# Performance work log

Hardware: AMD Instinct MI355X
Metric: run time of the kernel (lower is better)

## Reference

```python
import jax, jax.numpy as jnp
import numpy as np

N, C, MH, MW = 128, 256, 28, 28
K = 80          # num_classes
P = 196         # cfg.num_points
SH, SW = 200, 200  # stride-4 semantic feature map
STRIDE = 4.0
FC_IN = C + 2 * K  # 416


def _bilinear(feat, px, py):
    # feat: (C,H,W); px,py: (N,P) pixel coords. grid_sample semantics:
    # align_corners=False, zero padding.
    _, H, W = feat.shape
    x0 = jnp.floor(px); y0 = jnp.floor(py)
    wx1 = px - x0; wy1 = py - y0
    def corner(xc, yc, w):
        valid = (xc >= 0) & (xc <= W - 1) & (yc >= 0) & (yc <= H - 1)
        xi = jnp.clip(xc, 0, W - 1).astype(jnp.int32)
        yi = jnp.clip(yc, 0, H - 1).astype(jnp.int32)
        return feat[:, yi, xi] * (w * valid)[None]  # (C,N,P)
    out = (corner(x0, y0, (1 - wx1) * (1 - wy1)) + corner(x0 + 1, y0, wx1 * (1 - wy1))
           + corner(x0, y0 + 1, (1 - wx1) * wy1) + corner(x0 + 1, y0 + 1, wx1 * wy1))
    return jnp.transpose(out, (1, 0, 2))  # (N,C,P)


def setup_inputs():
    key = jax.random.key(0)
    ks = jax.random.split(key, 16)
    s = 0.02
    instance_feats = jax.random.normal(ks[0], (N, C, MH, MW), jnp.float32)
    semantic_feat = jax.random.normal(ks[1], (1, C, SH, SW), jnp.float32)
    img_w, img_h = SW * STRIDE, SH * STRIDE
    x1 = jax.random.uniform(ks[2], (N,)) * (img_w * 0.5)
    y1 = jax.random.uniform(ks[3], (N,)) * (img_h * 0.5)
    bw = 32.0 + jax.random.uniform(ks[4], (N,)) * (img_w * 0.4)
    bh = 32.0 + jax.random.uniform(ks[5], (N,)) * (img_h * 0.4)
    rois = jnp.stack([jnp.zeros((N,)), x1, y1,
                      jnp.minimum(x1 + bw, img_w - 1),
                      jnp.minimum(y1 + bh, img_h - 1)], axis=1)
    roi_labels = jax.random.randint(ks[6], (N,), 0, K)
    return dict(
        instance_feats=instance_feats, semantic_feat=semantic_feat, rois=rois,
        roi_labels=roi_labels, num_points=P,
        w_sem=s * jax.random.normal(ks[7], (C, C)), b_sem=jnp.zeros((C,)),
        w_inst=s * jax.random.normal(ks[8], (K, C)), b_inst=jnp.zeros((K,)),
        w_det=s * jax.random.normal(ks[9], (K, C)), b_det=jnp.zeros((K,)),
        fc_w0=s * jax.random.normal(ks[10], (C, FC_IN)), fc_b0=jnp.zeros((C,)),
        fc_w1=s * jax.random.normal(ks[11], (C, FC_IN)), fc_b1=jnp.zeros((C,)),
        fc_w2=s * jax.random.normal(ks[12], (C, FC_IN)), fc_b2=jnp.zeros((C,)),
        w_logits=s * jax.random.normal(ks[13], (C, FC_IN)), b_logits=jnp.zeros((C,)),
        w_fuse=s * jax.random.normal(ks[14], (C, C)), b_fuse=jnp.zeros((C,)))


def reference(instance_feats, semantic_feat, rois, roi_labels, num_points,
              w_sem, b_sem, w_inst, b_inst, w_det, b_det,
              fc_w0, fc_b0, fc_w1, fc_b1, fc_w2, fc_b2,
              w_logits, b_logits, w_fuse, b_fuse):
    n, c, mh, mw = instance_feats.shape
    hw = mh * mw
    sem = jax.nn.relu(jnp.einsum('bchw,oc->bohw', semantic_feat, w_sem) + b_sem[None, :, None, None])
    inst_log = jnp.einsum('nchw,oc->nohw', instance_feats, w_inst) + b_inst[None, :, None, None]
    det_log = jnp.einsum('nchw,oc->nohw', instance_feats, w_det) + b_det[None, :, None, None]
    ridx = jnp.arange(n)
    instance_preds = inst_log[ridx, roi_labels][:, None]  # (n,1,mh,mw) class-selected
    detail_preds = det_log[ridx, roi_labels][:, None]
    # top-k uncertain-point selection on the (detached) detail map
    point_map = jax.lax.stop_gradient(detail_preds.reshape(n, hw))
    _, point_indices = jax.lax.top_k(point_map, num_points)  # (n,P)
    rel_x = ((point_indices % mw).astype(jnp.float32) + 0.5) / mw
    rel_y = ((point_indices // mw).astype(jnp.float32) + 0.5) / mh
    # roi-relative [0,1]^2 -> semantic feature map pixel coords (align_corners=False)
    px = (rois[:, 1:2] + rel_x * (rois[:, 3:4] - rois[:, 1:2])) / STRIDE - 0.5
    py = (rois[:, 2:3] + rel_y * (rois[:, 4:5] - rois[:, 2:3])) / STRIDE - 0.5
    fine = _bilinear(sem[0], px, py)  # (n,C,P); all rois belong to image 0
    k = inst_log.shape[1]
    idx = jnp.broadcast_to(point_indices[:, None, :], (n, k, point_indices.shape[1]))
    c_inst = jnp.take_along_axis(inst_log.reshape(n, k, hw), idx, axis=2)  # (n,K,P)
    c_det = jnp.take_along_axis(det_log.reshape(n, k, hw), idx, axis=2)
    x = jnp.concatenate([fine, c_inst, c_det], axis=1)  # (n, C+2K, P)
    for w_, b_ in ((fc_w0, fc_b0), (fc_w1, fc_b1), (fc_w2, fc_b2)):
        x = jax.nn.relu(jnp.einsum('ncp,oc->nop', x, w_) + b_[None, :, None])
        x = jnp.concatenate([x, c_inst, c_det], axis=1)
    pts = jnp.einsum('ncp,oc->nop', x, w_logits) + b_logits[None, :, None]  # (n,C,P)
    coarse = instance_feats.reshape(n, c, hw)
    refined = coarse.at[ridx[:, None, None], jnp.arange(c)[None, :, None],
                        point_indices[:, None, :]].set(pts)
    refined = refined.reshape(n, c, mh, mw)
    fused = jax.nn.relu(jnp.einsum('nchw,oc->nohw', refined, w_fuse) + b_fuse[None, :, None, None])
    up = jax.image.resize(fused, (n, c, 2 * mh, 2 * mw), method='bilinear')
    return instance_preds, detail_preds, jax.nn.relu(up)
```

## Files before the change

### kernel.cpp

```cpp
#include <hip/hip_runtime.h>

#define NN   128
#define CC   256
#define MH   28
#define MW   28
#define HW   784
#define KCLS 80
#define PP   196
#define SHH  200
#define SWW  200
#define SPIX 40000
#define FCIN 416

typedef __attribute__((ext_vector_type(8))) short short8;
typedef __attribute__((ext_vector_type(4))) float f32x4;

__device__ __forceinline__ unsigned short f2bf(float x) {
  unsigned u = __float_as_uint(x);
  unsigned r = (u + 0x7fffu + ((u >> 16) & 1u)) >> 16;
  return (unsigned short)r;
}
__device__ __forceinline__ float bf2f(unsigned short h) {
  return __uint_as_float((unsigned)h << 16);
}

#define OW_SEM  0
#define OW_FUSE 65536
#define OW_FC0  131072
#define OW_FC1  237568
#define OW_FC2  344064
#define OW_LOG  450560
#define OW_CAT  557056
#define OW_TOT  598016
__global__ void wconv_k(const float* __restrict__ wsem, const float* __restrict__ wfuse,
                        const float* __restrict__ w0, const float* __restrict__ w1,
                        const float* __restrict__ w2, const float* __restrict__ wlog,
                        const float* __restrict__ wi, const float* __restrict__ wd,
                        const float* __restrict__ bi, const float* __restrict__ bd,
                        unsigned short* __restrict__ out, float* __restrict__ bcat) {
  const int tid0 = blockIdx.x * blockDim.x + threadIdx.x;
  if (tid0 < KCLS) bcat[tid0] = bi[tid0];
  else if (tid0 < 2 * KCLS) bcat[tid0] = bd[tid0 - KCLS];
  for (int i = tid0; i < OW_TOT; i += gridDim.x * blockDim.x) {
    float v;
    if (i < OW_FUSE) v = wsem[i];
    else if (i < OW_FC0) v = wfuse[i - OW_FUSE];
    else if (i < OW_FC1) v = w0[i - OW_FC0];
    else if (i < OW_FC2) v = w1[i - OW_FC1];
    else if (i < OW_LOG) v = w2[i - OW_FC2];
    else if (i < OW_CAT) v = wlog[i - OW_LOG];
    else if (i < OW_CAT + KCLS * 256) v = wi[i - OW_CAT];
    else v = wd[i - OW_CAT - KCLS * 256];
    out[i] = f2bf(v);
  }
}

__global__ __launch_bounds__(256) void transpose_bf16_k(
    const float* __restrict__ src, unsigned short* __restrict__ dst, int P) {
  __shared__ float T[64][69];
  const int t = threadIdx.x;
  src += (size_t)blockIdx.z * 256 * P;
  dst += (size_t)blockIdx.z * P * 256;
  const int p0 = blockIdx.x * 64, c0 = blockIdx.y * 64;
#pragma unroll
  for (int it = 0; it < 16; ++it) {
    int idx = it * 256 + t, c = idx >> 6, p = idx & 63;
    T[c][p] = (p0 + p < P) ? src[(size_t)(c0 + c) * P + p0 + p] : 0.f;
  }
  __syncthreads();
#pragma unroll
  for (int it = 0; it < 16; ++it) {
    int idx = it * 256 + t, p = idx >> 6, c = idx & 63;
    if (p0 + p < P) dst[(size_t)(p0 + p) * 256 + c0 + c] = f2bf(T[c][p]);
  }
}

template <int ASRC, int EPI>
__global__ __launch_bounds__(256) void gemm_mfma_k(
    const void* __restrict__ Ap, const unsigned short* __restrict__ Bmat,
    const float* __restrict__ bias, float* __restrict__ outf,
    unsigned short* __restrict__ outh, const int* __restrict__ pidx,
    int M, int N, int K, int lda, int ldb) {
  __shared__ __align__(16) unsigned short Abuf[128 * 40];
  __shared__ __align__(16) unsigned short Bbuf[128 * 40];
  const int t = threadIdx.x;
  const int m0 = blockIdx.x * 128, n0 = blockIdx.y * 128;
  if (EPI == 3) {
    Bmat += (size_t)blockIdx.z * HW * 256;
    outf += (size_t)blockIdx.z * CC * HW;
  }
  const unsigned short* Ah = (const unsigned short*)Ap;
  const int wave = t >> 6, lane = t & 63, lq = lane >> 4, lr = lane & 15;
  const int msub = (wave & 1) * 64, nsub = (wave >> 1) * 64;
  f32x4 acc[4][4] = {};
  for (int kc = 0; kc < K; kc += 32) {
#pragma unroll
    for (int it = 0; it < 4; ++it) {
      const int idx = it * 256 + t, r = idx >> 3, jg = idx & 7;
      const int gm = m0 + r;
      ushort4 h = make_ushort4(0, 0, 0, 0);
      if (gm < M) h = *(const ushort4*)&Ah[(size_t)gm * lda + kc + jg * 4];
      *(ushort4*)&Abuf[r * 40 + jg * 4] = h;
    }
#pragma unroll
    for (int it = 0; it < 4; ++it) {
      const int idx = it * 256 + t, r = idx >> 3, jg = idx & 7;
      const int gn = n0 + r;
      ushort4 h = make_ushort4(0, 0, 0, 0);
      if (gn < N) h = *(const ushort4*)&Bmat[(size_t)gn * ldb + kc + jg * 4];
      *(ushort4*)&Bbuf[r * 40 + jg * 4] = h;
    }
    __syncthreads();
    short8 af[4], bfr[4];
#pragma unroll
    for (int i = 0; i < 4; ++i)
      af[i] = *(const short8*)&Abuf[(msub + i * 16 + lr) * 40 + lq * 8];
#pragma unroll
    for (int f = 0; f < 4; ++f)
      bfr[f] = *(const short8*)&Bbuf[(nsub + f * 16 + lr) * 40 + lq * 8];
#pragma unroll
    for (int i = 0; i < 4; ++i)
#pragma unroll
      for (int f = 0; f < 4; ++f)
        acc[i][f] = __builtin_amdgcn_mfma_f32_16x16x32_bf16(af[i], bfr[f],
                                                            acc[i][f], 0, 0, 0);
    __syncthreads();
  }
#pragma unroll
  for (int i = 0; i < 4; ++i) {
#pragma unroll
    for (int r = 0; r < 4; ++r) {
      const int gm = m0 + msub + i * 16 + lq * 4 + r;
      if (EPI == 3) {
        const float bb = bias[gm];
#pragma unroll
        for (int f = 0; f < 4; ++f) {
          const int gs = n0 + nsub + f * 16 + lr;
          if (gs < N) outf[(size_t)gm * HW + gs] = fmaxf(acc[i][f][r] + bb, 0.f);
        }
      } else if (EPI == 4) {
        if (gm < M) {
#pragma unroll
          for (int f = 0; f < 4; ++f) {
            const int go = n0 + nsub + f * 16 + lr;
            outh[(size_t)gm * 256 + go] = f2bf(fmaxf(acc[i][f][r] + bias[go], 0.f));
          }
        }
      }
    }
  }
}

#define XRS 424
__global__ __launch_bounds__(256) void fused_point_k(
    const unsigned short* __restrict__ semh,
    unsigned short* __restrict__ refined_t,
    const int* __restrict__ pidx, const float* __restrict__ rois,
    const unsigned short* __restrict__ wbf, const float* __restrict__ bcat,
    const float* __restrict__ fb0, const float* __restrict__ fb1,
    const float* __restrict__ fb2, const float* __restrict__ bl) {
  __shared__ __align__(16) unsigned short X[64 * XRS];
  __shared__ int rowoff[64];
  __shared__ float pxs[64], pys[64];
  const int t = threadIdx.x;
  const int gm0 = blockIdx.x * 64;
  const int lane = t & 63, wave = t >> 6, lq = lane >> 4, lr = lane & 15;
  if (t < 64) {
    const int gm = gm0 + t;
    const int n = gm / PP;
    const int si = pidx[gm];
    rowoff[t] = (n * HW + si) * 256;
    const float rx = ((float)(si % MW) + 0.5f) / (float)MW;
    const float ry = ((float)(si / MW) + 0.5f) / (float)MH;
    const float x1 = rois[n * 5 + 1], y1 = rois[n * 5 + 2];
    const float x2 = rois[n * 5 + 3], y2 = rois[n * 5 + 4];
    pxs[t] = (x1 + rx * (x2 - x1)) * 0.25f - 0.5f;
    pys[t] = (y1 + ry * (y2 - y1)) * 0.25f - 0.5f;
  }
  __syncthreads();
  {
    const int c0 = (t & 31) * 8;
    const int rbase = t >> 5;
#pragma unroll
    for (int it = 0; it < 8; ++it) {
      const int r = it * 8 + rbase;
      const float px = pxs[r], py = pys[r];
      const float x0f = floorf(px), y0f = floorf(py);
      const int x0 = (int)x0f, y0 = (int)y0f;
      const float wx1 = px - x0f, wy1 = py - y0f;
      float out[8] = {};
#pragma unroll
      for (int cy = 0; cy < 2; ++cy) {
        const int yy = y0 + cy;
        const bool vy = (yy >= 0) && (yy <= SHH - 1);
        const int yc = min(max(yy, 0), SHH - 1);
        const float wy = cy ? wy1 : (1.f - wy1);
#pragma unroll
        for (int cx = 0; cx < 2; ++cx) {
          const int xx = x0 + cx;
          const bool vx = (xx >= 0) && (xx <= SWW - 1);
          const int xc = min(max(xx, 0), SWW - 1);
          const float wgt = (vx && vy) ? wy * (cx ? wx1 : (1.f - wx1)) : 0.f;
          const unsigned short* src = semh + ((size_t)yc * SWW + xc) * 256 + c0;
          short8 v = *(const short8*)src;
#pragma unroll
          for (int j = 0; j < 8; ++j) out[j] += wgt * bf2f((unsigned short)v[j]);
        }
      }
      short8 o;
#pragma unroll
      for (int j = 0; j < 8; ++j) o[j] = (short)f2bf(out[j]);
      *(short8*)&X[r * XRS + c0] = o;
    }
  }
  {
    const int grow = rowoff[wave * 16 + lr];
    const unsigned short* Wc = wbf + OW_CAT;
    f32x4 acc[10] = {};
    for (int kc = 0; kc < 256; kc += 32) {
      const short8 a = *(const short8*)&refined_t[(size_t)grow + kc + lq * 8];
#pragma unroll
      for (int f = 0; f < 10; ++f) {
        const short8 b = *(const short8*)&Wc[(size_t)(f * 16 + lr) * 256 + kc + lq * 8];
        acc[f] = __builtin_amdgcn_mfma_f32_16x16x32_bf16(a, b, acc[f], 0, 0, 0);
      }
    }
#pragma unroll
    for (int f = 0; f < 10; ++f) {
      const int col = 256 + f * 16 + lr;
      const float bb = bcat[f * 16 + lr];
#pragma unroll
      for (int r = 0; r < 4; ++r) {
        const int row = wave * 16 + lq * 4 + r;
        X[row * XRS + col] = f2bf(acc[f][r] + bb);
      }
    }
  }
  __syncthreads();
  const int n0w = wave * 64;
  for (int layer = 0; layer < 4; ++layer) {
    const unsigned short* Wl = wbf + OW_FC0 + layer * 106496;
    const float* bias = (layer == 0) ? fb0 : (layer == 1) ? fb1
                        : (layer == 2) ? fb2 : bl;
    f32x4 acc[4][4] = {};
#pragma unroll 2
    for (int kc = 0; kc < FCIN; kc += 32) {
      short8 af[4], bfr[4];
#pragma unroll
      for (int i = 0; i < 4; ++i)
        af[i] = *(const short8*)&X[(i * 16 + lr) * XRS + kc + lq * 8];
#pragma unroll
      for (int f = 0; f < 4; ++f)
        bfr[f] = *(const short8*)&Wl[(size_t)(n0w + f * 16 + lr) * FCIN + kc + lq * 8];
#pragma unroll
      for (int i = 0; i < 4; ++i)
#pragma unroll
        for (int f = 0; f < 4; ++f)
          acc[i][f] = __builtin_amdgcn_mfma_f32_16x16x32_bf16(af[i], bfr[f],
                                                              acc[i][f], 0, 0, 0);
    }
    __syncthreads();
    if (layer < 3) {
#pragma unroll
      for (int i = 0; i < 4; ++i)
#pragma unroll
        for (int r = 0; r < 4; ++r) {
          const int row = i * 16 + lq * 4 + r;
#pragma unroll
          for (int f = 0; f < 4; ++f) {
            const int col = n0w + f * 16 + lr;
            X[row * XRS + col] = f2bf(fmaxf(acc[i][f][r] + bias[col], 0.f));
          }
        }
    } else {
#pragma unroll
      for (int i = 0; i < 4; ++i)
#pragma unroll
        for (int r = 0; r < 4; ++r) {
          const int row = i * 16 + lq * 4 + r;
          unsigned short* dst = refined_t + (size_t)rowoff[row];
#pragma unroll
          for (int f = 0; f < 4; ++f) {
            const int col = n0w + f * 16 + lr;
            dst[col] = f2bf(acc[i][f][r] + bias[col]);
          }
        }
    }
    __syncthreads();
  }
}

__global__ __launch_bounds__(256) void select_maps_k(
    const float* __restrict__ inst, const int* __restrict__ labels,
    const float* __restrict__ w_inst, const float* __restrict__ b_inst,
    const float* __restrict__ w_det, const float* __restrict__ b_det,
    float* __restrict__ out0, float* __restrict__ out1) {
  const int n = blockIdx.x;
  const int s = blockIdx.y * 196 + threadIdx.x;
  if (threadIdx.x >= 196) return;
  const int lab = labels[n];
  const float* fi = inst + (size_t)n * CC * HW + s;
  const float* wi = w_inst + lab * 256;
  const float* wd = w_det + lab * 256;
  double ai = 0.0, ad = 0.0;
  for (int c = 0; c < 256; ++c) {
    const float v = fi[c * HW];
    ai += (double)v * (double)wi[c];
    ad += (double)v * (double)wd[c];
  }
  out0[n * HW + s] = (float)(ai + (double)b_inst[lab]);
  out1[n * HW + s] = (float)(ad + (double)b_det[lab]);
}

__global__ __launch_bounds__(256) void topk_k(const float* __restrict__ det,
                                              int* __restrict__ pidx) {
  __shared__ unsigned long long keys[1024];
  const int n = blockIdx.x;
  for (int i = threadIdx.x; i < 1024; i += 256) {
    unsigned long long kk = 0ull;
    if (i < HW) {
      unsigned u = __float_as_uint(det[n * HW + i]);
      u = (u & 0x80000000u) ? ~u : (u | 0x80000000u);
      kk = ((unsigned long long)u << 32) | (unsigned)(1023 - i);
    }
    keys[i] = kk;
  }
  __syncthreads();
  for (int k = 2; k <= 1024; k <<= 1) {
    for (int j = k >> 1; j > 0; j >>= 1) {
      for (int i = threadIdx.x; i < 1024; i += 256) {
        const int l = i ^ j;
        if (l > i) {
          const bool up = ((i & k) == 0);
          unsigned long long a = keys[i], bb = keys[l];
          if ((a > bb) == up) { keys[i] = bb; keys[l] = a; }
        }
      }
      __syncthreads();
    }
  }
  for (int r = threadIdx.x; r < PP; r += 256)
    pidx[n * PP + r] = 1023 - (int)(keys[828 + r] & 1023ull);
}

__global__ __launch_bounds__(256) void upsample_k(const float* __restrict__ fused,
                                                  float* __restrict__ out2) {
  __shared__ float L[HW];
  const int n = blockIdx.x, c = blockIdx.y;
  const float* src = fused + ((size_t)n * CC + c) * HW;
  for (int i = threadIdx.x; i < HW; i += 256) L[i] = src[i];
  __syncthreads();
  float* dst = out2 + ((size_t)n * CC + c) * 3136;
  for (int i = threadIdx.x; i < 3136; i += 256) {
    const int r = i / 56, q = i % 56;
    const float y = fminf(fmaxf(r * 0.5f - 0.25f, 0.f), 27.f);
    const float x = fminf(fmaxf(q * 0.5f - 0.25f, 0.f), 27.f);
    const int y0 = (int)y, x0 = (int)x;
    const float wy1 = y - (float)y0, wx1 = x - (float)x0;
    const int y1 = min(y0 + 1, 27), x1 = min(x0 + 1, 27);
    const float v00 = L[y0 * 28 + x0], v01 = L[y0 * 28 + x1];
    const float v10 = L[y1 * 28 + x0], v11 = L[y1 * 28 + x1];
    const float v = (1.f - wy1) * ((1.f - wx1) * v00 + wx1 * v01) +
                    wy1 * ((1.f - wx1) * v10 + wx1 * v11);
    dst[i] = fmaxf(v, 0.f);
  }
}

extern "C" void kernel_launch(void* const* d_in, const int* in_sizes, int n_in,
                              void* d_out, int out_size, void* d_ws, size_t ws_size,
                              hipStream_t stream) {
  (void)in_sizes; (void)n_in; (void)out_size; (void)ws_size;
  const float* inst   = (const float*)d_in[0];
  const float* semf   = (const float*)d_in[1];
  const float* rois   = (const float*)d_in[2];
  const int*   labels = (const int*)d_in[3];
  const float* w_sem  = (const float*)d_in[5];
  const float* b_sem  = (const float*)d_in[6];
  const float* w_inst = (const float*)d_in[7];
  const float* b_inst = (const float*)d_in[8];
  const float* w_det  = (const float*)d_in[9];
  const float* b_det  = (const float*)d_in[10];
  const float* fc_w0  = (const float*)d_in[11];
  const float* fc_b0  = (const float*)d_in[12];
  const float* fc_w1  = (const float*)d_in[13];
  const float* fc_b1  = (const float*)d_in[14];
  const float* fc_w2  = (const float*)d_in[15];
  const float* fc_b2  = (const float*)d_in[16];
  const float* w_log  = (const float*)d_in[17];
  const float* b_log  = (const float*)d_in[18];
  const float* w_fuse = (const float*)d_in[19];
  const float* b_fuse = (const float*)d_in[20];

  float* out0 = (float*)d_out;
  float* out1 = out0 + NN * HW;
  float* out2 = out0 + 2 * NN * HW;

  float* ws = (float*)d_ws;
  float* fused               = ws;
  int*   pidx                = (int*)(ws + 25690112);
  unsigned short* semh       = (unsigned short*)(ws + 25715200);
  unsigned short* semf_t     = (unsigned short*)(ws + 30835200);
  unsigned short* refined_t  = (unsigned short*)(ws + 35955200);
  unsigned short* wbf        = (unsigned short*)(ws + 48800256);
  float* bcat                = ws + 49099264;

  wconv_k<<<512, 256, 0, stream>>>(w_sem, w_fuse, fc_w0, fc_w1, fc_w2, w_log,
                                   w_inst, w_det, b_inst, b_det, wbf, bcat);
  transpose_bf16_k<<<dim3(625, 4, 1), 256, 0, stream>>>(semf, semf_t, SPIX);
  gemm_mfma_k<1, 4><<<dim3(313, 2, 1), 256, 0, stream>>>(
      semf_t, wbf + OW_SEM, b_sem, nullptr, semh, nullptr, SPIX, 256, 256, 256, 256);
  transpose_bf16_k<<<dim3(13, 4, NN), 256, 0, stream>>>(inst, refined_t, HW);
  select_maps_k<<<dim3(NN, 4), 256, 0, stream>>>(inst, labels, w_inst, b_inst,
                                                 w_det, b_det, out0, out1);
  topk_k<<<NN, 256, 0, stream>>>(out1, pidx);
  fused_point_k<<<392, 256, 0, stream>>>(semh, refined_t, pidx, rois, wbf, bcat,
                                         fc_b0, fc_b1, fc_b2, b_log);
  gemm_mfma_k<1, 3><<<dim3(2, 7, NN), 256, 0, stream>>>(
      wbf + OW_FUSE, refined_t, b_fuse, fused, nullptr, nullptr, 256, HW, 256, 256, 256);
  upsample_k<<<dim3(NN, CC), 256, 0, stream>>>(fused, out2);
}
```

Before: 845.9 us.

## Merge prep kernels into two megakernels and fuse fuse-conv GEMM with upsample

Weight conversion, both transposes and the label-selected channel reductions now run in one grid, with the reductions reusing the transposed tile in shared memory to write partial sums. The sem GEMM and the top-k sort share a second grid. The fuse 1x1 conv is now computed per 16-channel slab in shared memory and upsampled directly, so the fp32 fused intermediate no longer round-trips through global memory. This removes several launches and a second read of instance features, at the cost of more double-precision partial buffers and a less efficient fuse GEMM that reads B straight from global memory.

After: 827.4 us. 1.02x faster.

```diff
diff --git a/kernel.cpp b/kernel.cpp
--- a/kernel.cpp
+++ b/kernel.cpp
@@ -32,122 +32,194 @@
 #define OW_LOG  450560
 #define OW_CAT  557056
 #define OW_TOT  598016
-__global__ void wconv_k(const float* __restrict__ wsem, const float* __restrict__ wfuse,
-                        const float* __restrict__ w0, const float* __restrict__ w1,
-                        const float* __restrict__ w2, const float* __restrict__ wlog,
-                        const float* __restrict__ wi, const float* __restrict__ wd,
-                        const float* __restrict__ bi, const float* __restrict__ bd,
-                        unsigned short* __restrict__ out, float* __restrict__ bcat) {
-  const int tid0 = blockIdx.x * blockDim.x + threadIdx.x;
-  if (tid0 < KCLS) bcat[tid0] = bi[tid0];
-  else if (tid0 < 2 * KCLS) bcat[tid0] = bd[tid0 - KCLS];
-  for (int i = tid0; i < OW_TOT; i += gridDim.x * blockDim.x) {
-    float v;
-    if (i < OW_FUSE) v = wsem[i];
-    else if (i < OW_FC0) v = wfuse[i - OW_FUSE];
-    else if (i < OW_FC1) v = w0[i - OW_FC0];
-    else if (i < OW_FC2) v = w1[i - OW_FC1];
-    else if (i < OW_LOG) v = w2[i - OW_FC2];
-    else if (i < OW_CAT) v = wlog[i - OW_LOG];
-    else if (i < OW_CAT + KCLS * 256) v = wi[i - OW_CAT];
-    else v = wd[i - OW_CAT - KCLS * 256];
-    out[i] = f2bf(v);
-  }
-}
-
-__global__ __launch_bounds__(256) void transpose_bf16_k(
-    const float* __restrict__ src, unsigned short* __restrict__ dst, int P) {
+
+#define GA_SEMT 2500
+#define GA_INST 9156
+#define GA_TOT  9412
+__global__ __launch_bounds__(256) void megaA_k(
+    const float* __restrict__ semf, unsigned short* __restrict__ semf_t,
+    const float* __restrict__ inst, unsigned short* __restrict__ refined_t,
+    const int* __restrict__ labels,
+    const float* __restrict__ w_inst, const float* __restrict__ w_det,
+    double* __restrict__ Pb0, double* __restrict__ Pb1,
+    const float* __restrict__ wsem, const float* __restrict__ wfuse,
+    const float* __restrict__ w0, const float* __restrict__ w1,
+    const float* __restrict__ w2, const float* __restrict__ wlog,
+    const float* __restrict__ bi, const float* __restrict__ bd,
+    unsigned short* __restrict__ wbf, float* __restrict__ bcat) {
   __shared__ float T[64][69];
+  __shared__ double Dbi[4][65], Dbd[4][65];
+  const int bid = blockIdx.x;
   const int t = threadIdx.x;
-  src += (size_t)blockIdx.z * 256 * P;
-  dst += (size_t)blockIdx.z * P * 256;
-  const int p0 = blockIdx.x * 64, c0 = blockIdx.y * 64;
-#pragma unroll
-  for (int it = 0; it < 16; ++it) {
-    int idx = it * 256 + t, c = idx >> 6, p = idx & 63;
-    T[c][p] = (p0 + p < P) ? src[(size_t)(c0 + c) * P + p0 + p] : 0.f;
-  }
-  __syncthreads();
-#pragma unroll
-  for (int it = 0; it < 16; ++it) {
-    int idx = it * 256 + t, p = idx >> 6, c = idx & 63;
-    if (p0 + p < P) dst[(size_t)(p0 + p) * 256 + c0 + c] = f2bf(T[c][p]);
-  }
-}
-
-template <int ASRC, int EPI>
-__global__ __launch_bounds__(256) void gemm_mfma_k(
-    const void* __restrict__ Ap, const unsigned short* __restrict__ Bmat,
-    const float* __restrict__ bias, float* __restrict__ outf,
-    unsigned short* __restrict__ outh, const int* __restrict__ pidx,
-    int M, int N, int K, int lda, int ldb) {
-  __shared__ __align__(16) unsigned short Abuf[128 * 40];
-  __shared__ __align__(16) unsigned short Bbuf[128 * 40];
-  const int t = threadIdx.x;
-  const int m0 = blockIdx.x * 128, n0 = blockIdx.y * 128;
-  if (EPI == 3) {
-    Bmat += (size_t)blockIdx.z * HW * 256;
-    outf += (size_t)blockIdx.z * CC * HW;
-  }
-  const unsigned short* Ah = (const unsigned short*)Ap;
-  const int wave = t >> 6, lane = t & 63, lq = lane >> 4, lr = lane & 15;
-  const int msub = (wave & 1) * 64, nsub = (wave >> 1) * 64;
-  f32x4 acc[4][4] = {};
-  for (int kc = 0; kc < K; kc += 32) {
-#pragma unroll
-    for (int it = 0; it < 4; ++it) {
-      const int idx = it * 256 + t, r = idx >> 3, jg = idx & 7;
-      const int gm = m0 + r;
-      ushort4 h = make_ushort4(0, 0, 0, 0);
-      if (gm < M) h = *(const ushort4*)&Ah[(size_t)gm * lda + kc + jg * 4];
-      *(ushort4*)&Abuf[r * 40 + jg * 4] = h;
-    }
-#pragma unroll
-    for (int it = 0; it < 4; ++it) {
-      const int idx = it * 256 + t, r = idx >> 3, jg = idx & 7;
-      const int gn = n0 + r;
-      ushort4 h = make_ushort4(0, 0, 0, 0);
-      if (gn < N) h = *(const ushort4*)&Bmat[(size_t)gn * ldb + kc + jg * 4];
-      *(ushort4*)&Bbuf[r * 40 + jg * 4] = h;
+  if (bid < GA_INST) {
+    const bool isInst = (bid >= GA_SEMT);
+    int x, y, n, P;
+    const float* src;
+    unsigned short* dst;
+    if (!isInst) {
+      x = bid % 625; y = bid / 625; n = 0; P = SPIX;
+      src = semf; dst = semf_t;
+    } else {
+      const int b = bid - GA_SEMT;
+      n = b / 52; const int rr = b % 52; x = rr % 13; y = rr / 13; P = HW;
+      src = inst + (size_t)n * CC * HW;
+      dst = refined_t + (size_t)n * HW * 256;
+    }
+    const int p0 = x * 64, c0 = y * 64;
+#pragma unroll
+    for (int it = 0; it < 16; ++it) {
+      int idx = it * 256 + t, c = idx >> 6, p = idx & 63;
+      T[c][p] = (p0 + p < P) ? src[(size_t)(c0 + c) * P + p0 + p] : 0.f;
     }
     __syncthreads();
-    short8 af[4], bfr[4];
+#pragma unroll
+    for (int it = 0; it < 16; ++it) {
+      int idx = it * 256 + t, p = idx >> 6, c = idx & 63;
+      if (p0 + p < P) dst[(size_t)(p0 + p) * 256 + c0 + c] = f2bf(T[c][p]);
+    }
+    if (isInst) {
+      const int lab = labels[n];
+      const float* wi = w_inst + lab * 256 + c0;
+      const float* wd = w_det + lab * 256 + c0;
+      const int q = t >> 6, p = t & 63;
+      double si = 0.0, sd = 0.0;
+#pragma unroll
+      for (int j = 0; j < 16; ++j) {
+        const int c = q * 16 + j;
+        const double v = (double)T[c][p];
+        si += v * (double)wi[c];
+        sd += v * (double)wd[c];
+      }
+      Dbi[q][p] = si; Dbd[q][p] = sd;
+      __syncthreads();
+      if (t < 64 && p0 + t < HW) {
+        const double fi = ((Dbi[0][t] + Dbi[1][t]) + Dbi[2][t]) + Dbi[3][t];
+        const double fd = ((Dbd[0][t] + Dbd[1][t]) + Dbd[2][t]) + Dbd[3][t];
+        const size_t o = ((size_t)n * 4 + y) * HW + p0 + t;
+        Pb0[o] = fi; Pb1[o] = fd;
+      }
+    }
+  } else {
+    const int tid0 = (bid - GA_INST) * 256 + t;
+    if (tid0 < KCLS) bcat[tid0] = bi[tid0];
+    else if (tid0 < 2 * KCLS) bcat[tid0] = bd[tid0 - KCLS];
+    for (int i = tid0; i < OW_TOT; i += 256 * 256) {
+      float v;
+      if (i < OW_FUSE) v = wsem[i];
+      else if (i < OW_FC0) v = wfuse[i - OW_FUSE];
+      else if (i < OW_FC1) v = w0[i - OW_FC0];
+      else if (i < OW_FC2) v = w1[i - OW_FC1];
+      else if (i < OW_LOG) v = w2[i - OW_FC2];
+      else if (i < OW_CAT) v = wlog[i - OW_LOG];
+      else if (i < OW_CAT + KCLS * 256) v = w_inst[i - OW_CAT];
+      else v = w_det[i - OW_CAT - KCLS * 256];
+      wbf[i] = f2bf(v);
+    }
+  }
+}
+
+#define GB_GEMM 626
+#define GB_TOT  754
+__global__ __launch_bounds__(256) void megaB_k(
+    const unsigned short* __restrict__ semf_t, const unsigned short* __restrict__ wbf,
+    const float* __restrict__ b_sem, unsigned short* __restrict__ semh,
+    const double* __restrict__ Pb0, const double* __restrict__ Pb1,
+    const int* __restrict__ labels,
+    const float* __restrict__ b_inst, const float* __restrict__ b_det,
+    float* __restrict__ out0, float* __restrict__ out1, int* __restrict__ pidx) {
+  __shared__ __align__(16) unsigned char sm[20480];
+  const int bid = blockIdx.x, t = threadIdx.x;
+  if (bid < GB_GEMM) {
+    unsigned short* Abuf = (unsigned short*)sm;
+    unsigned short* Bbuf = (unsigned short*)(sm + 10240);
+    const int m0 = (bid % 313) * 128, n0 = (bid / 313) * 128;
+    const unsigned short* Bw = wbf + OW_SEM;
+    const int lane = t & 63, wave = t >> 6, lq = lane >> 4, lr = lane & 15;
+    const int msub = (wave & 1) * 64, nsub = (wave >> 1) * 64;
+    f32x4 acc[4][4] = {};
+    for (int kc = 0; kc < 256; kc += 32) {
+#pragma unroll
+      for (int it = 0; it < 4; ++it) {
+        const int idx = it * 256 + t, r = idx >> 3, jg = idx & 7;
+        const int gm = m0 + r;
+        ushort4 h = make_ushort4(0, 0, 0, 0);
+        if (gm < SPIX) h = *(const ushort4*)&semf_t[(size_t)gm * 256 + kc + jg * 4];
+        *(ushort4*)&Abuf[r * 40 + jg * 4] = h;
+      }
+#pragma unroll
+      for (int it = 0; it < 4; ++it) {
+        const int idx = it * 256 + t, r = idx >> 3, jg = idx & 7;
+        const int gn = n0 + r;
+        ushort4 h = make_ushort4(0, 0, 0, 0);
+        if (gn < 256) h = *(const ushort4*)&Bw[(size_t)gn * 256 + kc + jg * 4];
+        *(ushort4*)&Bbuf[r * 40 + jg * 4] = h;
+      }
+      __syncthreads();
+      short8 af[4], bfr[4];
+#pragma unroll
+      for (int i = 0; i < 4; ++i)
+        af[i] = *(const short8*)&Abuf[(msub + i * 16 + lr) * 40 + lq * 8];
+#pragma unroll
+      for (int f = 0; f < 4; ++f)
+        bfr[f] = *(const short8*)&Bbuf[(nsub + f * 16 + lr) * 40 + lq * 8];
+#pragma unroll
+      for (int i = 0; i < 4; ++i)
+#pragma unroll
+        for (int f = 0; f < 4; ++f)
+          acc[i][f] = __builtin_amdgcn_mfma_f32_16x16x32_bf16(af[i], bfr[f],
+                                                              acc[i][f], 0, 0, 0);
+      __syncthreads();
+    }
 #pragma unroll
     for (int i = 0; i < 4; ++i)
-      af[i] = *(const short8*)&Abuf[(msub + i * 16 + lr) * 40 + lq * 8];
-#pragma unroll
-    for (int f = 0; f < 4; ++f)
-      bfr[f] = *(const short8*)&Bbuf[(nsub + f * 16 + lr) * 40 + lq * 8];
-#pragma unroll
-    for (int i = 0; i < 4; ++i)
-#pragma unroll
-      for (int f = 0; f < 4; ++f)
-        acc[i][f] = __builtin_amdgcn_mfma_f32_16x16x32_bf16(af[i], bfr[f],
-                                                            acc[i][f], 0, 0, 0);
-    __syncthreads();
-  }
-#pragma unroll
-  for (int i = 0; i < 4; ++i) {
-#pragma unroll
-    for (int r = 0; r < 4; ++r) {
-      const int gm = m0 + msub + i * 16 + lq * 4 + r;
-      if (EPI == 3) {
-        const float bb = bias[gm];
-#pragma unroll
-        for (int f = 0; f < 4; ++f) {
-          const int gs = n0 + nsub + f * 16 + lr;
-          if (gs < N) outf[(size_t)gm * HW + gs] = fmaxf(acc[i][f][r] + bb, 0.f);
-        }
-      } else if (EPI == 4) {
-        if (gm < M) {
+#pragma unroll
+      for (int r = 0; r < 4; ++r) {
+        const int gm = m0 + msub + i * 16 + lq * 4 + r;
+        if (gm < SPIX) {
 #pragma unroll
           for (int f = 0; f < 4; ++f) {
             const int go = n0 + nsub + f * 16 + lr;
-            outh[(size_t)gm * 256 + go] = f2bf(fmaxf(acc[i][f][r] + bias[go], 0.f));
+            semh[(size_t)gm * 256 + go] = f2bf(fmaxf(acc[i][f][r] + b_sem[go], 0.f));
           }
         }
       }
-    }
+  } else {
+    unsigned long long* keys = (unsigned long long*)sm;
+    const int n = bid - GB_GEMM;
+    const int lab = labels[n];
+    const double bdi = (double)b_inst[lab], bdd = (double)b_det[lab];
+    for (int i = t; i < 1024; i += 256) {
+      unsigned long long kk = 0ull;
+      if (i < HW) {
+        const size_t base = (size_t)n * 4 * HW + i;
+        const double fi = ((Pb0[base] + Pb0[base + HW]) + Pb0[base + 2 * HW]) + Pb0[base + 3 * HW];
+        const double fd = ((Pb1[base] + Pb1[base + HW]) + Pb1[base + 2 * HW]) + Pb1[base + 3 * HW];
+        const float vi = (float)(fi + bdi);
+        const float vd = (float)(fd + bdd);
+        out0[n * HW + i] = vi;
+        out1[n * HW + i] = vd;
+        unsigned u = __float_as_uint(vd);
+        u = (u & 0x80000000u) ? ~u : (u | 0x80000000u);
+        kk = ((unsigned long long)u << 32) | (unsigned)(1023 - i);
+      }
+      keys[i] = kk;
+    }
+    __syncthreads();
+    for (int k = 2; k <= 1024; k <<= 1) {
+      for (int j = k >> 1; j > 0; j >>= 1) {
+        for (int i = t; i < 1024; i += 256) {
+          const int l = i ^ j;
+          if (l > i) {
+            const bool up = ((i & k) == 0);
+            unsigned long long a = keys[i], bb = keys[l];
+            if ((a > bb) == up) { keys[i] = bb; keys[l] = a; }
+          }
+        }
+        __syncthreads();
+      }
+    }
+    for (int r = t; r < PP; r += 256)
+      pidx[n * PP + r] = 1023 - (int)(keys[828 + r] & 1023ull);
   }
 }
 
@@ -290,79 +362,62 @@
   }
 }
 
-__global__ __launch_bounds__(256) void select_maps_k(
-    const float* __restrict__ inst, const int* __restrict__ labels,
-    const float* __restrict__ w_inst, const float* __restrict__ b_inst,
-    const float* __restrict__ w_det, const float* __restrict__ b_det,
-    float* __restrict__ out0, float* __restrict__ out1) {
-  const int n = blockIdx.x;
-  const int s = blockIdx.y * 196 + threadIdx.x;
-  if (threadIdx.x >= 196) return;
-  const int lab = labels[n];
-  const float* fi = inst + (size_t)n * CC * HW + s;
-  const float* wi = w_inst + lab * 256;
-  const float* wd = w_det + lab * 256;
-  double ai = 0.0, ad = 0.0;
-  for (int c = 0; c < 256; ++c) {
-    const float v = fi[c * HW];
-    ai += (double)v * (double)wi[c];
-    ad += (double)v * (double)wd[c];
-  }
-  out0[n * HW + s] = (float)(ai + (double)b_inst[lab]);
-  out1[n * HW + s] = (float)(ad + (double)b_det[lab]);
-}
-
-__global__ __launch_bounds__(256) void topk_k(const float* __restrict__ det,
-                                              int* __restrict__ pidx) {
-  __shared__ unsigned long long keys[1024];
-  const int n = blockIdx.x;
-  for (int i = threadIdx.x; i < 1024; i += 256) {
-    unsigned long long kk = 0ull;
-    if (i < HW) {
-      unsigned u = __float_as_uint(det[n * HW + i]);
-      u = (u & 0x80000000u) ? ~u : (u | 0x80000000u);
-      kk = ((unsigned long long)u << 32) | (unsigned)(1023 - i);
-    }
-    keys[i] = kk;
-  }
+__global__ __launch_bounds__(256) void fuse_up_k(
+    const unsigned short* __restrict__ refined_t, const unsigned short* __restrict__ wbf,
+    const float* __restrict__ b_fuse, float* __restrict__ out2) {
+  __shared__ __align__(16) unsigned short Abuf[16 * 268];
+  __shared__ float Fbuf[16 * 788];
+  const int t = threadIdx.x;
+  const int bx = blockIdx.x & 15, n = blockIdx.x >> 4;
+  const int lane = t & 63, wave = t >> 6, lq = lane >> 4, lr = lane & 15;
+#pragma unroll
+  for (int it = 0; it < 2; ++it) {
+    const int u = it * 256 + t;
+    const int row = u >> 5, col8 = (u & 31) * 8;
+    *(short8*)&Abuf[row * 268 + col8] =
+        *(const short8*)&wbf[OW_FUSE + ((bx * 16 + row) << 8) + col8];
+  }
+  const unsigned short* Bn = refined_t + (size_t)n * HW * 256;
   __syncthreads();
-  for (int k = 2; k <= 1024; k <<= 1) {
-    for (int j = k >> 1; j > 0; j >>= 1) {
-      for (int i = threadIdx.x; i < 1024; i += 256) {
-        const int l = i ^ j;
-        if (l > i) {
-          const bool up = ((i & k) == 0);
-          unsigned long long a = keys[i], bb = keys[l];
-          if ((a > bb) == up) { keys[i] = bb; keys[l] = a; }
-        }
-      }
-      __syncthreads();
-    }
-  }
-  for (int r = threadIdx.x; r < PP; r += 256)
-    pidx[n * PP + r] = 1023 - (int)(keys[828 + r] & 1023ull);
-}
-
-__global__ __launch_bounds__(256) void upsample_k(const float* __restrict__ fused,
-                                                  float* __restrict__ out2) {
-  __shared__ float L[HW];
-  const int n = blockIdx.x, c = blockIdx.y;
-  const float* src = fused + ((size_t)n * CC + c) * HW;
-  for (int i = threadIdx.x; i < HW; i += 256) L[i] = src[i];
+  f32x4 acc[13] = {};
+  for (int kc = 0; kc < 256; kc += 32) {
+    const short8 a = *(const short8*)&Abuf[lr * 268 + kc + lq * 8];
+#pragma unroll
+    for (int f = 0; f < 13; ++f) {
+      const int s = (wave * 13 + f) * 16 + lr;
+      const int sc = (s < HW) ? s : 0;
+      const short8 b = *(const short8*)&Bn[(size_t)sc * 256 + kc + lq * 8];
+      acc[f] = __builtin_amdgcn_mfma_f32_16x16x32_bf16(a, b, acc[f], 0, 0, 0);
+    }
+  }
+#pragma unroll
+  for (int f = 0; f < 13; ++f) {
+    const int s = (wave * 13 + f) * 16 + lr;
+    if (s < HW) {
+#pragma unroll
+      for (int r = 0; r < 4; ++r) {
+        const int cl = lq * 4 + r;
+        Fbuf[cl * 788 + s] = fmaxf(acc[f][r] + b_fuse[bx * 16 + cl], 0.f);
+      }
+    }
+  }
   __syncthreads();
-  float* dst = out2 + ((size_t)n * CC + c) * 3136;
-  for (int i = threadIdx.x; i < 3136; i += 256) {
-    const int r = i / 56, q = i % 56;
-    const float y = fminf(fmaxf(r * 0.5f - 0.25f, 0.f), 27.f);
-    const float x = fminf(fmaxf(q * 0.5f - 0.25f, 0.f), 27.f);
-    const int y0 = (int)y, x0 = (int)x;
-    const float wy1 = y - (float)y0, wx1 = x - (float)x0;
-    const int y1 = min(y0 + 1, 27), x1 = min(x0 + 1, 27);
-    const float v00 = L[y0 * 28 + x0], v01 = L[y0 * 28 + x1];
-    const float v10 = L[y1 * 28 + x0], v11 = L[y1 * 28 + x1];
-    const float v = (1.f - wy1) * ((1.f - wx1) * v00 + wx1 * v01) +
-                    wy1 * ((1.f - wx1) * v10 + wx1 * v11);
-    dst[i] = fmaxf(v, 0.f);
+  float* dst = out2 + ((size_t)(n * CC + bx * 16)) * 3136;
+  for (int cl = 0; cl < 16; ++cl) {
+    const float* L = &Fbuf[cl * 788];
+    for (int j = t; j < 3136; j += 256) {
+      const int r = j / 56, q = j % 56;
+      const float y = fminf(fmaxf(r * 0.5f - 0.25f, 0.f), 27.f);
+      const float x = fminf(fmaxf(q * 0.5f - 0.25f, 0.f), 27.f);
+      const int y0 = (int)y, x0 = (int)x;
+      const float wy1 = y - (float)y0, wx1 = x - (float)x0;
+      const int y1 = min(y0 + 1, 27), x1 = min(x0 + 1, 27);
+      const float v00 = L[y0 * 28 + x0], v01 = L[y0 * 28 + x1];
+      const float v10 = L[y1 * 28 + x0], v11 = L[y1 * 28 + x1];
+      const float v = (1.f - wy1) * ((1.f - wx1) * v00 + wx1 * v01) +
+                      wy1 * ((1.f - wx1) * v10 + wx1 * v11);
+      dst[(size_t)cl * 3136 + j] = fmaxf(v, 0.f);
+    }
   }
 }
 
@@ -396,26 +451,22 @@
   float* out2 = out0 + 2 * NN * HW;
 
   float* ws = (float*)d_ws;
-  float* fused               = ws;
-  int*   pidx                = (int*)(ws + 25690112);
-  unsigned short* semh       = (unsigned short*)(ws + 25715200);
-  unsigned short* semf_t     = (unsigned short*)(ws + 30835200);
-  unsigned short* refined_t  = (unsigned short*)(ws + 35955200);
-  unsigned short* wbf        = (unsigned short*)(ws + 48800256);
-  float* bcat                = ws + 49099264;
-
-  wconv_k<<<512, 256, 0, stream>>>(w_sem, w_fuse, fc_w0, fc_w1, fc_w2, w_log,
-                                   w_inst, w_det, b_inst, b_det, wbf, bcat);
-  transpose_bf16_k<<<dim3(625, 4, 1), 256, 0, stream>>>(semf, semf_t, SPIX);
-  gemm_mfma_k<1, 4><<<dim3(313, 2, 1), 256, 0, stream>>>(
-      semf_t, wbf + OW_SEM, b_sem, nullptr, semh, nullptr, SPIX, 256, 256, 256, 256);
-  transpose_bf16_k<<<dim3(13, 4, NN), 256, 0, stream>>>(inst, refined_t, HW);
-  select_maps_k<<<dim3(NN, 4), 256, 0, stream>>>(inst, labels, w_inst, b_inst,
-                                                 w_det, b_det, out0, out1);
-  topk_k<<<NN, 256, 0, stream>>>(out1, pidx);
+  int*   pidx               = (int*)ws;
+  unsigned short* semh      = (unsigned short*)(ws + 25088);
+  unsigned short* semf_t    = (unsigned short*)(ws + 5145088);
+  unsigned short* refined_t = (unsigned short*)(ws + 10265088);
+  unsigned short* wbf       = (unsigned short*)(ws + 23110144);
+  float* bcat               = ws + 23409152;
+  double* Pb0               = (double*)(ws + 23409312);
+  double* Pb1               = (double*)(ws + 24212128);
+
+  megaA_k<<<GA_TOT, 256, 0, stream>>>(semf, semf_t, inst, refined_t, labels,
+                                      w_inst, w_det, Pb0, Pb1,
+                                      w_sem, w_fuse, fc_w0, fc_w1, fc_w2, w_log,
+                                      b_inst, b_det, wbf, bcat);
+  megaB_k<<<GB_TOT, 256, 0, stream>>>(semf_t, wbf, b_sem, semh, Pb0, Pb1, labels,
+                                      b_inst, b_det, out0, out1, pidx);
   fused_point_k<<<392, 256, 0, stream>>>(semh, refined_t, pidx, rois, wbf, bcat,
                                          fc_b0, fc_b1, fc_b2, b_log);
-  gemm_mfma_k<1, 3><<<dim3(2, 7, NN), 256, 0, stream>>>(
-      wbf + OW_FUSE, refined_t, b_fuse, fused, nullptr, nullptr, 256, HW, 256, 256, 256);
-  upsample_k<<<dim3(NN, CC), 256, 0, stream>>>(fused, out2);
-}
+  fuse_up_k<<<NN * 16, 256, 0, stream>>>(refined_t, wbf, b_fuse, out2);
+}
```
